# Kernel tuning notes

Hardware: AMD Instinct MI355X
Metric: run time of the kernel (lower is better)

The kernel has to match this reference:

```python
import jax, jax.numpy as jnp
import numpy as np


def _maxpool3d(x, s=2):
    # MaxPool3d(kernel_size=s) -> stride=s, VALID padding
    return jax.lax.reduce_window(x, -jnp.inf, jax.lax.max,
                                 (1, 1, s, s, s), (1, 1, s, s, s), 'VALID')


def _spectral_norm(W, u):
    # W: [out_c, in_c]. One power iteration with u/v detached, matching
    # torch.nn.utils.spectral_norm's training-step behavior.
    v = W.T @ u
    v = v / (jnp.linalg.norm(v) + 1e-12)
    u2 = W @ v
    u2 = u2 / (jnp.linalg.norm(u2) + 1e-12)
    u2 = jax.lax.stop_gradient(u2)
    v = jax.lax.stop_gradient(v)
    sigma = u2 @ (W @ v)
    return W / sigma


def setup_inputs() -> dict:
    key = jax.random.key(0)
    ks = jax.random.split(key, 6)
    B, C, D = 4, 256, 32
    kc, vc, oc = 128, 128, 256
    return {
        'x':  jax.random.normal(ks[0], (B, C, D, D, D), jnp.float32),
        'Wk': jax.random.normal(ks[1], (kc, C), jnp.float32) * 0.05,  # shared f_key/f_query 1x1x1 conv
        'bk': jnp.zeros((kc,), jnp.float32),
        'Wv': jax.random.normal(ks[2], (vc, C), jnp.float32) * 0.05,  # f_value 1x1x1 conv
        'bv': jnp.zeros((vc,), jnp.float32),
        'Ww': jax.random.normal(ks[3], (oc, vc), jnp.float32) * 0.05,  # output W 1x1x1 conv
        'bw': jnp.zeros((oc,), jnp.float32),
        'u':  jax.random.normal(ks[4], (kc,), jnp.float32),            # spectral-norm power-iter vector
    }


def reference(x, Wk, bk, Wv, bv, Ww, bw, u):
    B, C = x.shape[0], x.shape[1]
    kc = Wk.shape[0]
    xp = _maxpool3d(x, 2)                      # [B,C,16,16,16]
    sp = xp.shape[2:]
    N = sp[0] * sp[1] * sp[2]                  # 4096 flattened positions
    xf = xp.reshape(B, C, N)                   # [B,C,N]

    Wq = _spectral_norm(Wk, u)                 # f_query = f_key (shared weights)
    q = jnp.einsum('kc,bcn->bnk', Wq, xf) + bk                    # [B,N,kc]
    k = jnp.einsum('kc,bcn->bkn', Wq, xf) + bk[None, :, None]     # [B,kc,N]
    v = jnp.einsum('vc,bcn->bnv', Wv, xf) + bv                    # [B,N,vc]

    sim = jnp.einsum('bnk,bkm->bnm', q, k) * (kc ** -0.5)         # [B,N,N]
    attn = jax.nn.softmax(sim, axis=-1)
    ctx = jnp.einsum('bnm,bmv->bnv', attn, v)                     # [B,N,vc]

    out = jnp.einsum('ov,bnv->bon', Ww, ctx) + bw[None, :, None]  # [B,oc,N]
    return out.reshape(B, Ww.shape[0], *sp)    # [B,oc,16,16,16] (pooled spatial, as in original)
```

## Files before the change

kernel.cpp:

```cpp
#include <hip/hip_runtime.h>

typedef __attribute__((ext_vector_type(8))) short short8;
typedef __attribute__((ext_vector_type(4))) float f32x4;
typedef __attribute__((ext_vector_type(16))) float f32x16;

static constexpr size_t OFF_SIGMA = 0;
static constexpr size_t OFF_ML    = 256;
static constexpr size_t OFF_QKT   = 1048576;
static constexpr size_t OFF_V     = OFF_QKT + 4194304;
static constexpr size_t OFF_WCAT  = OFF_V + 4194304;
static constexpr size_t OFF_XFB   = OFF_WCAT + 196608;
static constexpr size_t OFF_PC    = OFF_XFB;

__device__ inline unsigned short f2bf(float f) {
  unsigned int u = __float_as_uint(f);
  unsigned int r = u + 0x7fffu + ((u >> 16) & 1u);
  return (unsigned short)(r >> 16);
}
__device__ inline float bf2f(unsigned short s) {
  return __uint_as_float(((unsigned int)s) << 16);
}
__device__ inline unsigned int cvtpk_bf16(float a, float b) {
  unsigned int r;
  asm("v_cvt_pk_bf16_f32 %0, %1, %2" : "=v"(r) : "v"(a), "v"(b));
  return r;
}

__launch_bounds__(256)
__global__ void k_maxpool(const float* __restrict__ x, unsigned short* __restrict__ xfb) {
  int idx = blockIdx.x * 256 + threadIdx.x;
  int n2 = idx & 2047;
  int bc = idx >> 11;
  int d2p = n2 & 7, d1 = (n2 >> 3) & 15, d0 = n2 >> 7;
  const float* p = x + (size_t)bc * 32768 + (size_t)d0 * 2048 + d1 * 64 + d2p * 4;
  float4 a = *(const float4*)(p);
  float4 b = *(const float4*)(p + 32);
  float4 c = *(const float4*)(p + 1024);
  float4 e = *(const float4*)(p + 1056);
  float o0 = fmaxf(fmaxf(fmaxf(a.x, a.y), fmaxf(b.x, b.y)),
                   fmaxf(fmaxf(c.x, c.y), fmaxf(e.x, e.y)));
  float o1 = fmaxf(fmaxf(fmaxf(a.z, a.w), fmaxf(b.z, b.w)),
                   fmaxf(fmaxf(c.z, c.w), fmaxf(e.z, e.w)));
  unsigned int pk = (unsigned int)f2bf(o0) | ((unsigned int)f2bf(o1) << 16);
  *(unsigned int*)(xfb + (size_t)bc * 4096 + n2 * 2) = pk;
}

__global__ void k_sigma(const float* __restrict__ Wk, const float* __restrict__ u,
                        float* __restrict__ sig) {
  __shared__ float vsh[256];
  __shared__ float red[256];
  __shared__ float ush[128];
  int t = threadIdx.x;
  if (t < 128) ush[t] = u[t];
  __syncthreads();
  float acc = 0.f;
  for (int k = 0; k < 128; k++) acc += Wk[(size_t)k * 256 + t] * ush[k];
  vsh[t] = acc;
  red[t] = acc * acc;
  __syncthreads();
  for (int s = 128; s > 0; s >>= 1) { if (t < s) red[t] += red[t + s]; __syncthreads(); }
  float nrm = sqrtf(red[0]) + 1e-12f;
  float vn = vsh[t] / nrm;
  __syncthreads();
  vsh[t] = vn;
  __syncthreads();
  float acc2 = 0.f;
  if (t < 128) {
    for (int c = 0; c < 256; c++) acc2 += Wk[(size_t)t * 256 + c] * vsh[c];
  }
  red[t] = (t < 128) ? acc2 * acc2 : 0.f;
  __syncthreads();
  for (int s = 128; s > 0; s >>= 1) { if (t < s) red[t] += red[t + s]; __syncthreads(); }
  if (t == 0) {
    float s2v = red[0];
    sig[0] = s2v / (sqrtf(s2v) + 1e-12f);
  }
}

__launch_bounds__(256)
__global__ void k_prep(const float* __restrict__ Ww, const float* __restrict__ Wk,
                       const float* __restrict__ Wv, unsigned short* __restrict__ wcat) {
  int i = (blockIdx.x * 256 + threadIdx.x) * 4;
  const float* src = (i < 32768) ? (Ww + i) : (i < 65536) ? (Wk + i - 32768)
                                                          : (Wv + i - 65536);
  float4 w = *(const float4*)src;
  unsigned int lo = (unsigned int)f2bf(w.x) | ((unsigned int)f2bf(w.y) << 16);
  unsigned int hi = (unsigned int)f2bf(w.z) | ((unsigned int)f2bf(w.w) << 16);
  *(uint2*)(wcat + i) = make_uint2(lo, hi);
}

__launch_bounds__(256)
__global__ void k_qkv(const unsigned short* __restrict__ xfb,
                      const unsigned short* __restrict__ wcat,
                      const float* __restrict__ bk, const float* __restrict__ bv,
                      const float* __restrict__ sig,
                      unsigned short* __restrict__ qkT, unsigned short* __restrict__ vws) {
  __shared__ __align__(16) unsigned short Bl[64 * 64];
  int bid = blockIdx.x;
  int nt = bid & 63, b = bid >> 6;
  int n0 = nt * 64;
  int t = threadIdx.x, wid = t >> 6, lane = t & 63, g = lane >> 4, lr = lane & 15;
  int R0 = wid * 64;
  bool isq = (wid < 2);
  const unsigned short* wb = isq ? (wcat + 32768 + (size_t)R0 * 256)
                                 : (wcat + 65536 + (size_t)(R0 - 128) * 256);
  f32x4 acc[4][4];
#pragma unroll
  for (int i = 0; i < 4; i++)
#pragma unroll
    for (int j = 0; j < 4; j++) acc[i][j] = (f32x4){0.f, 0.f, 0.f, 0.f};

  short8 st[2];
#pragma unroll
  for (int i = 0; i < 2; i++) {
    int gid = i * 256 + t;
    st[i] = *(const short8*)(xfb + ((size_t)(b * 256 + (gid >> 3))) * 4096 +
                             n0 + (gid & 7) * 8);
  }

#pragma unroll 1
  for (int ks4 = 0; ks4 < 4; ks4++) {
    int k0 = ks4 * 64;
    __syncthreads();
#pragma unroll
    for (int i = 0; i < 2; i++) {
      int gid = i * 256 + t;
      int c = gid >> 3, nch = gid & 7;
#pragma unroll
      for (int j = 0; j < 8; j++) {
        int n = nch * 8 + j;
        Bl[n * 64 + (((c >> 3) ^ (n & 7)) << 3) + (c & 7)] = (unsigned short)st[i][j];
      }
    }
    if (ks4 < 3) {
#pragma unroll
      for (int i = 0; i < 2; i++) {
        int gid = i * 256 + t;
        st[i] = *(const short8*)(xfb + ((size_t)(b * 256 + k0 + 64 + (gid >> 3))) * 4096 +
                                 n0 + (gid & 7) * 8);
      }
    }
    __syncthreads();
#pragma unroll
    for (int ks2 = 0; ks2 < 2; ks2++) {
      short8 af[4], bf[4];
#pragma unroll
      for (int ot = 0; ot < 4; ot++)
        af[ot] = *(const short8*)(wb + (size_t)(ot * 16 + lr) * 256 + k0 + ks2 * 32 + g * 8);
#pragma unroll
      for (int nt2 = 0; nt2 < 4; nt2++) {
        int n = nt2 * 16 + lr;
        bf[nt2] = *(const short8*)(Bl + n * 64 + (((ks2 * 4 + g) ^ (n & 7)) << 3));
      }
#pragma unroll
      for (int ot = 0; ot < 4; ot++)
#pragma unroll
        for (int nt2 = 0; nt2 < 4; nt2++)
          acc[ot][nt2] = __builtin_amdgcn_mfma_f32_16x16x32_bf16(af[ot], bf[nt2],
                                                                 acc[ot][nt2], 0, 0, 0);
    }
  }

  if (isq) {
    float inv_s = 1.0f / sig[0];
#pragma unroll
    for (int ot = 0; ot < 4; ot++)
#pragma unroll
      for (int rr = 0; rr < 4; rr++) {
        int d = R0 + ot * 16 + g * 4 + rr;
        float bias = bk[d];
#pragma unroll
        for (int nt2 = 0; nt2 < 4; nt2++) {
          int n = n0 + nt2 * 16 + lr;
          float val = acc[ot][nt2][rr] * inv_s + bias;
          int ds = ((((d >> 3) ^ (n & 7)) & 15) << 3) | (d & 7);
          qkT[((size_t)b * 4096 + n) * 128 + ds] = f2bf(val);
        }
      }
  } else {
#pragma unroll
    for (int ot = 0; ot < 4; ot++)
#pragma unroll
      for (int rr = 0; rr < 4; rr++) {
        int d = R0 - 128 + ot * 16 + g * 4 + rr;
        float bias = bv[d];
#pragma unroll
        for (int nt2 = 0; nt2 < 4; nt2++) {
          int n = n0 + nt2 * 16 + lr;
          int c = n & 63;
          int cs = ((((c >> 3) ^ (d & 7)) & 7) << 3) | (c & 7);
          vws[((size_t)(b * 128 + d)) * 4096 + (n & ~63) + cs] =
              f2bf(acc[ot][nt2][rr] + bias);
        }
      }
  }
}

__launch_bounds__(256, 2)
__global__ void k_attn(const unsigned short* __restrict__ qkT,
                       const unsigned short* __restrict__ vws,
                       unsigned short* __restrict__ pc, float* __restrict__ lsum) {
  __shared__ __align__(16) char smem[2][32768];
  const float C1 = 0.12751744f;
  int p = blockIdx.x;
  int bid = (p & 7) * 128 + (p >> 3);
  int sp = bid & 7, qt = (bid >> 3) & 31, b = bid >> 8;
  int kv0 = sp * 512;
  int t = threadIdx.x, wid = t >> 6, lane = t & 63;
  int l31 = lane & 31, hi = lane >> 5;
  int qrb = qt * 128 + wid * 32;
  const unsigned short* qk_b = qkT + (size_t)b * 524288;
  const char* kgb = (const char*)qk_b;
  const char* vgb = (const char*)(vws + (size_t)b * 524288);

  bool stk = (wid < 2);
  int ch0 = (wid & 1) * 8;
  const char* vsrc_base = vgb + (size_t)(lane >> 3) * 8192 + (lane & 7) * 16;

#define STAGE(BUF, MB)                                                         \
  {                                                                            \
    char* base_ = smem[BUF];                                                   \
    _Pragma("unroll")                                                          \
    for (int i_ = 0; i_ < 8; i_++) {                                           \
      int ch_ = ch0 + i_;                                                      \
      if (stk) {                                                               \
        const char* g_ = kgb + (size_t)(MB) * 256 + ch_ * 1024 + lane * 16;    \
        __builtin_amdgcn_global_load_lds(                                      \
            (const __attribute__((address_space(1))) unsigned int*)g_,         \
            (__attribute__((address_space(3))) unsigned int*)(base_ + ch_ * 1024), \
            16, 0, 0);                                                         \
      } else {                                                                 \
        const char* g_ = vsrc_base + (size_t)ch_ * 65536 + (size_t)(MB) * 2;   \
        __builtin_amdgcn_global_load_lds(                                      \
            (const __attribute__((address_space(1))) unsigned int*)g_,         \
            (__attribute__((address_space(3))) unsigned int*)(base_ + 16384 + ch_ * 1024), \
            16, 0, 0);                                                         \
      }                                                                        \
    }                                                                          \
  }

  STAGE(0, kv0)

  short8 qf[8];
  {
    int row = qrb + l31;
    const unsigned short* qr = qk_b + (size_t)row * 128;
#pragma unroll
    for (int kk = 0; kk < 8; kk++)
      qf[kk] = *(const short8*)(qr + (((2 * kk + hi) ^ (row & 7)) << 3));
  }

  f32x16 acc[4];
#pragma unroll
  for (int dt = 0; dt < 4; dt++)
#pragma unroll
    for (int r = 0; r < 16; r++) acc[dt][r] = 0.f;
  float lacc = 0.f;

  __syncthreads();

#pragma unroll 1
  for (int it = 0; it < 8; ++it) {
    int cur = it & 1;
    if (it < 7) STAGE(cur ^ 1, kv0 + it * 64 + 64)
    const char* KL = smem[cur];
    const char* VL = smem[cur] + 16384;

    f32x16 s0, s1;
#pragma unroll
    for (int r = 0; r < 16; r++) { s0[r] = 0.f; s1[r] = 0.f; }
    __builtin_amdgcn_s_setprio(1);
#pragma unroll
    for (int kk = 0; kk < 8; kk++) {
      int cs = 2 * kk + hi;
      short8 kf0 = *(const short8*)(KL + l31 * 256 + ((cs ^ (l31 & 7)) << 4));
      short8 kf1 = *(const short8*)(KL + (32 + l31) * 256 + ((cs ^ (l31 & 7)) << 4));
      s0 = __builtin_amdgcn_mfma_f32_32x32x16_bf16(kf0, qf[kk], s0, 0, 0, 0);
      s1 = __builtin_amdgcn_mfma_f32_32x32x16_bf16(kf1, qf[kk], s1, 0, 0, 0);
    }
    __builtin_amdgcn_s_setprio(0);

    short8 pa[4];
#pragma unroll
    for (int ct = 0; ct < 2; ct++) {
      unsigned int w0[4], w1[4];
#pragma unroll
      for (int a = 0; a < 4; a++) {
        float v0 = ct ? s1[4 * a + 0] : s0[4 * a + 0];
        float v1 = ct ? s1[4 * a + 1] : s0[4 * a + 1];
        float v2 = ct ? s1[4 * a + 2] : s0[4 * a + 2];
        float v3 = ct ? s1[4 * a + 3] : s0[4 * a + 3];
        float p0 = __builtin_amdgcn_exp2f(v0 * C1);
        float p1 = __builtin_amdgcn_exp2f(v1 * C1);
        float p2 = __builtin_amdgcn_exp2f(v2 * C1);
        float p3 = __builtin_amdgcn_exp2f(v3 * C1);
        lacc += (p0 + p1) + (p2 + p3);
        w0[a] = cvtpk_bf16(p0, p1);
        w1[a] = cvtpk_bf16(p2, p3);
      }
#pragma unroll
      for (int k2 = 0; k2 < 2; k2++) {
        unsigned int xa = w0[2 * k2], ya = w0[2 * k2 + 1];
        unsigned int xb = w1[2 * k2], yb = w1[2 * k2 + 1];
        asm("v_permlane32_swap_b32 %0, %1" : "+v"(xa), "+v"(ya));
        asm("v_permlane32_swap_b32 %0, %1" : "+v"(xb), "+v"(yb));
        union { unsigned int u[4]; short8 s8; } pk_;
        pk_.u[0] = xa; pk_.u[1] = xb; pk_.u[2] = ya; pk_.u[3] = yb;
        pa[ct * 2 + k2] = pk_.s8;
      }
    }

    __builtin_amdgcn_s_setprio(1);
#pragma unroll
    for (int ks = 0; ks < 4; ks++) {
      int cv = 2 * ks + hi;
#pragma unroll
      for (int dt = 0; dt < 4; dt++) {
        int d = dt * 32 + l31;
        short8 vb = *(const short8*)(VL + d * 128 + ((cv ^ (d & 7)) << 4));
        acc[dt] = __builtin_amdgcn_mfma_f32_32x32x16_bf16(pa[ks], vb, acc[dt], 0, 0, 0);
      }
    }
    __builtin_amdgcn_s_setprio(0);
    __syncthreads();
  }

  float lf = lacc + __shfl_xor(lacc, 32);

  char* OL = smem[0] + wid * 8704;
#pragma unroll
  for (int dt = 0; dt < 4; dt++)
#pragma unroll
    for (int r = 0; r < 16; r++) {
      int q = (r & 3) + 8 * (r >> 2) + 4 * hi;
      *(unsigned short*)(OL + q * 272 + (dt * 32 + l31) * 2) = f2bf(acc[dt][r]);
    }
  unsigned short* dst = pc + ((size_t)sp * 16384 + (size_t)b * 4096 + qrb) * 128;
#pragma unroll
  for (int j = 0; j < 8; j++) {
    int row = lane >> 1;
    int off = (lane & 1) * 128 + j * 16;
    short8 v = *(const short8*)(OL + row * 272 + off);
    *(short8*)((char*)dst + row * 256 + off) = v;
  }
  if (lane < 32) lsum[sp * 16384 + (size_t)b * 4096 + qrb + l31] = lf;
#undef STAGE
}

__launch_bounds__(256)
__global__ void k_mergeout(const unsigned short* __restrict__ pc,
                           const float* __restrict__ lsum,
                           const unsigned short* __restrict__ wwb,
                           const float* __restrict__ bw,
                           float* __restrict__ out) {
  __shared__ float inv_l[64];
  __shared__ __align__(16) unsigned short Bl[64 * 128];
  int bid = blockIdx.x;
  int nt = bid & 63, b = bid >> 6;
  int n0 = nt * 64;
  size_t gnb = (size_t)b * 4096 + n0;
  int t = threadIdx.x;

  if (t < 64) {
    float L = 0.f;
#pragma unroll
    for (int sp = 0; sp < 8; sp++) L += lsum[sp * 16384 + gnb + t];
    inv_l[t] = 1.f / L;
  }
  __syncthreads();

  {
    int n = t & 63, vs = t >> 6;
    float o[32] = {};
#pragma unroll
    for (int sp = 0; sp < 8; sp++) {
      const unsigned short* src = pc + ((size_t)sp * 16384 + gnb + n) * 128 + vs * 32;
#pragma unroll
      for (int c = 0; c < 4; c++) {
        short8 pv = *(const short8*)(src + c * 8);
#pragma unroll
        for (int j = 0; j < 8; j++) o[c * 8 + j] += bf2f((unsigned short)pv[j]);
      }
    }
    float inv = inv_l[n];
    unsigned int* B32 = (unsigned int*)Bl;
#pragma unroll
    for (int jj = 0; jj < 16; jj++) {
      int v = vs * 32 + jj * 2;
      int kg = v >> 3;
      int kgp = (kg & 8) | ((kg ^ n) & 7);
      unsigned int pk = (unsigned int)f2bf(o[jj * 2] * inv) |
                        ((unsigned int)f2bf(o[jj * 2 + 1] * inv) << 16);
      B32[n * 64 + kgp * 4 + ((v & 7) >> 1)] = pk;
    }
  }
  __syncthreads();

  int wid = t >> 6, lane = t & 63, g = lane >> 4, lr = lane & 15;
  int o0 = wid * 64;
  short8 af[4][4];
#pragma unroll
  for (int ot = 0; ot < 4; ot++) {
    int o = o0 + ot * 16 + lr;
#pragma unroll
    for (int ks = 0; ks < 4; ks++)
      af[ot][ks] = *(const short8*)(wwb + (size_t)o * 128 + ks * 32 + g * 8);
  }
  f32x4 acc[4][4];
#pragma unroll
  for (int i = 0; i < 4; i++)
#pragma unroll
    for (int j = 0; j < 4; j++) acc[i][j] = (f32x4){0.f, 0.f, 0.f, 0.f};
#pragma unroll
  for (int nt2 = 0; nt2 < 4; nt2++) {
    short8 bfr[4];
#pragma unroll
    for (int ks = 0; ks < 4; ks++) {
      int kg = ks * 4 + g;
      int kgp = (kg & 8) | ((kg ^ lr) & 7);
      bfr[ks] = *(const short8*)(Bl + (nt2 * 16 + lr) * 128 + kgp * 8);
    }
#pragma unroll
    for (int ot = 0; ot < 4; ot++)
#pragma unroll
      for (int ks = 0; ks < 4; ks++)
        acc[ot][nt2] = __builtin_amdgcn_mfma_f32_16x16x32_bf16(af[ot][ks], bfr[ks],
                                                               acc[ot][nt2], 0, 0, 0);
  }
#pragma unroll
  for (int ot = 0; ot < 4; ot++)
#pragma unroll
    for (int r = 0; r < 4; r++) {
      int o = o0 + ot * 16 + g * 4 + r;
      float bias = bw[o];
#pragma unroll
      for (int nt2 = 0; nt2 < 4; nt2++)
        out[((size_t)(b * 256 + o)) * 4096 + n0 + nt2 * 16 + lr] = acc[ot][nt2][r] + bias;
    }
}

extern "C" void kernel_launch(void* const* d_in, const int* in_sizes, int n_in,
                              void* d_out, int out_size, void* d_ws, size_t ws_size,
                              hipStream_t stream) {
  const float* x  = (const float*)d_in[0];
  const float* Wk = (const float*)d_in[1];
  const float* bk = (const float*)d_in[2];
  const float* Wv = (const float*)d_in[3];
  const float* bv = (const float*)d_in[4];
  const float* Ww = (const float*)d_in[5];
  const float* bw = (const float*)d_in[6];
  const float* u  = (const float*)d_in[7];

  char* ws = (char*)d_ws;
  float* sig            = (float*)(ws + OFF_SIGMA);
  float* lsum           = (float*)(ws + OFF_ML);
  unsigned short* qkT   = (unsigned short*)(ws + OFF_QKT);
  unsigned short* vbuf  = (unsigned short*)(ws + OFF_V);
  unsigned short* wcat  = (unsigned short*)(ws + OFF_WCAT);
  unsigned short* xfb   = (unsigned short*)(ws + OFF_XFB);
  unsigned short* pc    = (unsigned short*)(ws + OFF_PC);
  float* out            = (float*)d_out;

  k_maxpool<<<8192, 256, 0, stream>>>(x, xfb);
  k_sigma<<<1, 256, 0, stream>>>(Wk, u, sig);
  k_prep<<<96, 256, 0, stream>>>(Ww, Wk, Wv, wcat);
  k_qkv<<<256, 256, 0, stream>>>(xfb, wcat, bk, bv, sig, qkT, vbuf);
  k_attn<<<1024, 256, 0, stream>>>(qkT, vbuf, pc, lsum);
  k_mergeout<<<256, 256, 0, stream>>>(pc, lsum, wcat, bw, out);
}
```

Measured before the change: 109.6 us.

## Fuse maxpool into QKV projection, merge init kernels, halve attention KV splits

The separate maxpool kernel is removed. The 2x2x2 max-pooling and the bf16 conversion now happen while the QKV projection kernel loads x, so the pooled intermediate is never written to or read back from global memory. The sigma power iteration and the weight bf16 conversion are merged into one launch, and sigma reads a transposed Wk from LDS instead of making strided global reads. Attention now uses 4 KV splits instead of 8, which halves the blocks and the partial-context merge traffic but leaves fewer blocks to fill the GPU. A risk is that the 256-block QKV kernel now carries all of the x reads, which lowers the parallelism applied to the largest memory read.

```diff
diff --git a/kernel.cpp b/kernel.cpp
--- a/kernel.cpp
+++ b/kernel.cpp
@@ -9,8 +9,7 @@
 static constexpr size_t OFF_QKT   = 1048576;
 static constexpr size_t OFF_V     = OFF_QKT + 4194304;
 static constexpr size_t OFF_WCAT  = OFF_V + 4194304;
-static constexpr size_t OFF_XFB   = OFF_WCAT + 196608;
-static constexpr size_t OFF_PC    = OFF_XFB;
+static constexpr size_t OFF_PC    = OFF_WCAT + 196608;
 
 __device__ inline unsigned short f2bf(float f) {
   unsigned int u = __float_as_uint(f);
@@ -27,34 +26,36 @@
 }
 
 __launch_bounds__(256)
-__global__ void k_maxpool(const float* __restrict__ x, unsigned short* __restrict__ xfb) {
-  int idx = blockIdx.x * 256 + threadIdx.x;
-  int n2 = idx & 2047;
-  int bc = idx >> 11;
-  int d2p = n2 & 7, d1 = (n2 >> 3) & 15, d0 = n2 >> 7;
-  const float* p = x + (size_t)bc * 32768 + (size_t)d0 * 2048 + d1 * 64 + d2p * 4;
-  float4 a = *(const float4*)(p);
-  float4 b = *(const float4*)(p + 32);
-  float4 c = *(const float4*)(p + 1024);
-  float4 e = *(const float4*)(p + 1056);
-  float o0 = fmaxf(fmaxf(fmaxf(a.x, a.y), fmaxf(b.x, b.y)),
-                   fmaxf(fmaxf(c.x, c.y), fmaxf(e.x, e.y)));
-  float o1 = fmaxf(fmaxf(fmaxf(a.z, a.w), fmaxf(b.z, b.w)),
-                   fmaxf(fmaxf(c.z, c.w), fmaxf(e.z, e.w)));
-  unsigned int pk = (unsigned int)f2bf(o0) | ((unsigned int)f2bf(o1) << 16);
-  *(unsigned int*)(xfb + (size_t)bc * 4096 + n2 * 2) = pk;
-}
-
-__global__ void k_sigma(const float* __restrict__ Wk, const float* __restrict__ u,
-                        float* __restrict__ sig) {
+__global__ void k_init(const float* __restrict__ Ww, const float* __restrict__ Wk,
+                       const float* __restrict__ Wv, const float* __restrict__ u,
+                       unsigned short* __restrict__ wcat, float* __restrict__ sig) {
+  __shared__ float WT[256][129];
+  __shared__ float red[256];
   __shared__ float vsh[256];
-  __shared__ float red[256];
   __shared__ float ush[128];
   int t = threadIdx.x;
+  if (blockIdx.x < 96) {
+    int i = (blockIdx.x * 256 + t) * 4;
+    const float* src = (i < 32768) ? (Ww + i) : (i < 65536) ? (Wk + i - 32768)
+                                                            : (Wv + i - 65536);
+    float4 w = *(const float4*)src;
+    unsigned int lo = (unsigned int)f2bf(w.x) | ((unsigned int)f2bf(w.y) << 16);
+    unsigned int hi = (unsigned int)f2bf(w.z) | ((unsigned int)f2bf(w.w) << 16);
+    *(uint2*)(wcat + i) = make_uint2(lo, hi);
+    return;
+  }
+#pragma unroll
+  for (int i = 0; i < 32; i++) {
+    int idx = i * 1024 + t * 4;
+    float4 w = *(const float4*)(Wk + idx);
+    int k = idx >> 8, c = idx & 255;
+    WT[c][k] = w.x; WT[c + 1][k] = w.y; WT[c + 2][k] = w.z; WT[c + 3][k] = w.w;
+  }
   if (t < 128) ush[t] = u[t];
   __syncthreads();
   float acc = 0.f;
-  for (int k = 0; k < 128; k++) acc += Wk[(size_t)k * 256 + t] * ush[k];
+#pragma unroll 8
+  for (int k = 0; k < 128; k++) acc += WT[t][k] * ush[k];
   vsh[t] = acc;
   red[t] = acc * acc;
   __syncthreads();
@@ -66,7 +67,8 @@
   __syncthreads();
   float acc2 = 0.f;
   if (t < 128) {
-    for (int c = 0; c < 256; c++) acc2 += Wk[(size_t)t * 256 + c] * vsh[c];
+#pragma unroll 8
+    for (int c = 0; c < 256; c++) acc2 += WT[c][t] * vsh[c];
   }
   red[t] = (t < 128) ? acc2 * acc2 : 0.f;
   __syncthreads();
@@ -78,19 +80,7 @@
 }
 
 __launch_bounds__(256)
-__global__ void k_prep(const float* __restrict__ Ww, const float* __restrict__ Wk,
-                       const float* __restrict__ Wv, unsigned short* __restrict__ wcat) {
-  int i = (blockIdx.x * 256 + threadIdx.x) * 4;
-  const float* src = (i < 32768) ? (Ww + i) : (i < 65536) ? (Wk + i - 32768)
-                                                          : (Wv + i - 65536);
-  float4 w = *(const float4*)src;
-  unsigned int lo = (unsigned int)f2bf(w.x) | ((unsigned int)f2bf(w.y) << 16);
-  unsigned int hi = (unsigned int)f2bf(w.z) | ((unsigned int)f2bf(w.w) << 16);
-  *(uint2*)(wcat + i) = make_uint2(lo, hi);
-}
-
-__launch_bounds__(256)
-__global__ void k_qkv(const unsigned short* __restrict__ xfb,
+__global__ void k_qkv(const float* __restrict__ x,
                       const unsigned short* __restrict__ wcat,
                       const float* __restrict__ bk, const float* __restrict__ bv,
                       const float* __restrict__ sig,
@@ -110,36 +100,42 @@
 #pragma unroll
     for (int j = 0; j < 4; j++) acc[i][j] = (f32x4){0.f, 0.f, 0.f, 0.f};
 
-  short8 st[2];
-#pragma unroll
-  for (int i = 0; i < 2; i++) {
-    int gid = i * 256 + t;
-    st[i] = *(const short8*)(xfb + ((size_t)(b * 256 + (gid >> 3))) * 4096 +
-                             n0 + (gid & 7) * 8);
-  }
+  int cc = t >> 2, q4 = t & 3;
+  int d0p = n0 >> 8;
+  int d1p = ((n0 >> 4) & 15) + q4;
+  const float* xrow = x + ((size_t)(b * 256) << 15) + d0p * 2048 + d1p * 64;
+
+  unsigned short pool[16];
+#define POOLLOAD(C)                                                          \
+  {                                                                          \
+    const float* pr_ = xrow + (size_t)(C) * 32768;                           \
+    _Pragma("unroll")                                                        \
+    for (int k8 = 0; k8 < 8; k8++) {                                         \
+      float4 a_ = *(const float4*)(pr_ + k8 * 4);                            \
+      float4 b_ = *(const float4*)(pr_ + 32 + k8 * 4);                       \
+      float4 c_ = *(const float4*)(pr_ + 1024 + k8 * 4);                     \
+      float4 d_ = *(const float4*)(pr_ + 1056 + k8 * 4);                     \
+      float p0_ = fmaxf(fmaxf(fmaxf(a_.x, a_.y), fmaxf(b_.x, b_.y)),         \
+                        fmaxf(fmaxf(c_.x, c_.y), fmaxf(d_.x, d_.y)));        \
+      float p1_ = fmaxf(fmaxf(fmaxf(a_.z, a_.w), fmaxf(b_.z, b_.w)),         \
+                        fmaxf(fmaxf(c_.z, c_.w), fmaxf(d_.z, d_.w)));        \
+      pool[k8 * 2] = f2bf(p0_);                                              \
+      pool[k8 * 2 + 1] = f2bf(p1_);                                          \
+    }                                                                        \
+  }
+
+  POOLLOAD(cc)
 
 #pragma unroll 1
   for (int ks4 = 0; ks4 < 4; ks4++) {
     int k0 = ks4 * 64;
     __syncthreads();
 #pragma unroll
-    for (int i = 0; i < 2; i++) {
-      int gid = i * 256 + t;
-      int c = gid >> 3, nch = gid & 7;
-#pragma unroll
-      for (int j = 0; j < 8; j++) {
-        int n = nch * 8 + j;
-        Bl[n * 64 + (((c >> 3) ^ (n & 7)) << 3) + (c & 7)] = (unsigned short)st[i][j];
-      }
-    }
-    if (ks4 < 3) {
-#pragma unroll
-      for (int i = 0; i < 2; i++) {
-        int gid = i * 256 + t;
-        st[i] = *(const short8*)(xfb + ((size_t)(b * 256 + k0 + 64 + (gid >> 3))) * 4096 +
-                                 n0 + (gid & 7) * 8);
-      }
-    }
+    for (int j = 0; j < 16; j++) {
+      int nn = q4 * 16 + j;
+      Bl[nn * 64 + (((cc >> 3) ^ (nn & 7)) << 3) + (cc & 7)] = pool[j];
+    }
+    if (ks4 < 3) POOLLOAD(k0 + 64 + cc)
     __syncthreads();
 #pragma unroll
     for (int ks2 = 0; ks2 < 2; ks2++) {
@@ -160,6 +156,7 @@
                                                                  acc[ot][nt2], 0, 0, 0);
     }
   }
+#undef POOLLOAD
 
   if (isq) {
     float inv_s = 1.0f / sig[0];
@@ -203,9 +200,9 @@
   __shared__ __align__(16) char smem[2][32768];
   const float C1 = 0.12751744f;
   int p = blockIdx.x;
-  int bid = (p & 7) * 128 + (p >> 3);
-  int sp = bid & 7, qt = (bid >> 3) & 31, b = bid >> 8;
-  int kv0 = sp * 512;
+  int bid = (p & 7) * 64 + (p >> 3);
+  int sp = bid & 3, qt = (bid >> 2) & 31, b = bid >> 7;
+  int kv0 = sp * 1024;
   int t = threadIdx.x, wid = t >> 6, lane = t & 63;
   int l31 = lane & 31, hi = lane >> 5;
   int qrb = qt * 128 + wid * 32;
@@ -260,9 +257,9 @@
   __syncthreads();
 
 #pragma unroll 1
-  for (int it = 0; it < 8; ++it) {
+  for (int it = 0; it < 16; ++it) {
     int cur = it & 1;
-    if (it < 7) STAGE(cur ^ 1, kv0 + it * 64 + 64)
+    if (it < 15) STAGE(cur ^ 1, kv0 + it * 64 + 64)
     const char* KL = smem[cur];
     const char* VL = smem[cur] + 16384;
 
@@ -364,7 +361,7 @@
   if (t < 64) {
     float L = 0.f;
 #pragma unroll
-    for (int sp = 0; sp < 8; sp++) L += lsum[sp * 16384 + gnb + t];
+    for (int sp = 0; sp < 4; sp++) L += lsum[sp * 16384 + gnb + t];
     inv_l[t] = 1.f / L;
   }
   __syncthreads();
@@ -373,7 +370,7 @@
     int n = t & 63, vs = t >> 6;
     float o[32] = {};
 #pragma unroll
-    for (int sp = 0; sp < 8; sp++) {
+    for (int sp = 0; sp < 4; sp++) {
       const unsigned short* src = pc + ((size_t)sp * 16384 + gnb + n) * 128 + vs * 32;
 #pragma unroll
       for (int c = 0; c < 4; c++) {
@@ -457,14 +454,11 @@
   unsigned short* qkT   = (unsigned short*)(ws + OFF_QKT);
   unsigned short* vbuf  = (unsigned short*)(ws + OFF_V);
   unsigned short* wcat  = (unsigned short*)(ws + OFF_WCAT);
-  unsigned short* xfb   = (unsigned short*)(ws + OFF_XFB);
   unsigned short* pc    = (unsigned short*)(ws + OFF_PC);
   float* out            = (float*)d_out;
 
-  k_maxpool<<<8192, 256, 0, stream>>>(x, xfb);
-  k_sigma<<<1, 256, 0, stream>>>(Wk, u, sig);
-  k_prep<<<96, 256, 0, stream>>>(Ww, Wk, Wv, wcat);
-  k_qkv<<<256, 256, 0, stream>>>(xfb, wcat, bk, bv, sig, qkT, vbuf);
-  k_attn<<<1024, 256, 0, stream>>>(qkT, vbuf, pc, lsum);
+  k_init<<<97, 256, 0, stream>>>(Ww, Wk, Wv, u, wcat, sig);
+  k_qkv<<<256, 256, 0, stream>>>(x, wcat, bk, bv, sig, qkT, vbuf);
+  k_attn<<<512, 256, 0, stream>>>(qkT, vbuf, pc, lsum);
   k_mergeout<<<256, 256, 0, stream>>>(pc, lsum, wcat, bw, out);
 }
```

Result: faster. 101.0 us (-7.9%).
